# Kernel optimization log

Hardware: AMD Instinct MI355X
Metric: run time of the kernel (lower is better)

Reference implementation:

```python
import jax, jax.numpy as jnp
import numpy as np

B = 8       # number of point clouds
N = 4096    # points per cloud (start_point)
M = 1024    # sampled points per cloud (sampled_point_ammount), ratio 0.25
D = 64      # feature dim


def setup_inputs() -> dict:
    key = jax.random.key(0)
    k1, k2 = jax.random.split(key)
    x = jax.random.normal(k1, (B * N, D), dtype=jnp.float32)
    pos = jax.random.uniform(k2, (B * N, 3), dtype=jnp.float32)
    batch = jnp.repeat(jnp.arange(B, dtype=jnp.int32), N)  # sorted batch ids
    return {"x": x, "pos": pos, "batch": batch}


def _fps_single(pos_b, m):
    # Farthest point sampling on one cloud [N,3]; deterministic start at index 0.
    n = pos_b.shape[0]
    big = jnp.asarray(jnp.finfo(pos_b.dtype).max, pos_b.dtype)

    def step(carry, _):
        mind, last = carry
        d = jnp.sum((pos_b - pos_b[last]) ** 2, axis=-1)  # [N]
        mind = jnp.minimum(mind, d)
        nxt = jnp.argmax(mind).astype(jnp.int32)
        return (mind, nxt), nxt

    init = (jnp.full((n,), big, pos_b.dtype), jnp.int32(0))
    _, rest = jax.lax.scan(step, init, None, length=m - 1)
    return jnp.concatenate([jnp.zeros((1,), jnp.int32), rest])  # [M]


def reference(x, pos, batch):
    pos_b = pos.reshape(B, N, 3)
    # --- DownsampleMRG: FPS gather (scale_factor = M/N) ---
    idx = jax.vmap(lambda p: _fps_single(p, M))(pos_b)              # [B, M] local idx
    gidx = (idx + jnp.arange(B, dtype=jnp.int32)[:, None] * N).reshape(-1)
    x_lr = x[gidx]                                                  # [B*M, D]
    pos_lr = pos[gidx]                                              # [B*M, 3]
    # --- UpsampleMRG: lr_x = cat([x_lr, pos_lr]); knn_interpolate k=1 ---
    lr_feat = jnp.concatenate([x_lr, pos_lr], axis=1).reshape(B, M, D + 3)
    pos_lr_b = pos_lr.reshape(B, M, 3)
    # pairwise squared distances hr->lr within each cloud: [B, N, M]
    d2 = jnp.sum((pos_b[:, :, None, :] - pos_lr_b[:, None, :, :]) ** 2, axis=-1)
    nn = jnp.argmin(d2, axis=-1)                                    # [B, N]
    # k=1 interpolation: weights normalize to 1 -> pure nearest-neighbor gather
    interp = jnp.take_along_axis(lr_feat, nn[:, :, None], axis=1).reshape(B * N, D + 3)
    # out_x = cat([x_hr, pos_hr, interpolated lr features])
    out_x = jnp.concatenate([x, pos, interp], axis=1)               # [B*N, D+3+D+3]
    return out_x, jnp.zeros((out_x.shape[0], 3), pos.dtype), batch
```

## Files before the change

### kernel.cpp

```cpp
#include <hip/hip_runtime.h>
#include <cstdint>

#define BATCH 8
#define NPTS  4096
#define MPTS  1024
#define DIM   64

typedef float v2f __attribute__((ext_vector_type(2)));
typedef unsigned long long u64;
typedef unsigned int u32;

__device__ __forceinline__ double mk_key(float m, u32 aux) {
  const u64 k = ((u64)__float_as_uint(m) << 32) | (u64)aux;
  return __longlong_as_double((long long)k);
}
__device__ __forceinline__ u32 key_lo(double d) {
  return (u32)(u64)__double_as_longlong(d);
}

#define WAVE_MAX_F64_STEP(x, ctrl)                                                    \
  {                                                                                   \
    const u64 xu_ = (u64)__double_as_longlong(x);                                     \
    const int lo_ = __builtin_amdgcn_update_dpp(0, (int)(u32)xu_, (ctrl), 0xf, 0xf, true);  \
    const int hi_ = __builtin_amdgcn_update_dpp(0, (int)(u32)(xu_ >> 32), (ctrl), 0xf, 0xf, true); \
    const double y_ = __longlong_as_double((long long)(((u64)(u32)hi_ << 32) | (u64)(u32)lo_)); \
    (x) = fmax((x), y_);                                                              \
  }

__global__ __launch_bounds__(256) void fps_kernel(const float* __restrict__ pos,
                                                  int* __restrict__ gidx) {
#pragma clang fp contract(off)
  const int b = blockIdx.x;
  const int t = threadIdx.x;
  const float* p = pos + (size_t)b * NPTS * 3;

  __shared__ float4 sp[NPTS];
  __shared__ double red[2][4];

  v2f px[8], py[8], pz[8], mind[8];
#pragma unroll
  for (int k = 0; k < 16; ++k) {
    const int i = t + k * 256;
    const float a = p[3 * i + 0];
    const float c = p[3 * i + 1];
    const float d = p[3 * i + 2];
    sp[i] = make_float4(a, c, d, 0.0f);
    px[k >> 1][k & 1] = a;
    py[k >> 1][k & 1] = c;
    pz[k >> 1][k & 1] = d;
    mind[k >> 1][k & 1] = 3.402823466e+38f;
  }
  __syncthreads();

  float4 w = sp[0];
  float lx = w.x, ly = w.y, lz = w.z;

  int h0 = 0, h1 = 0, h2 = 0, h3 = 0;
  const int it1 = t + 256, it2 = t + 512, it3 = t + 768;

  for (int it = 1; it < MPTS; ++it) {
    const v2f vlx = {lx, lx}, vly = {ly, ly}, vlz = {lz, lz};
    double pg[8];
#pragma unroll
    for (int g = 0; g < 8; ++g) {
      const v2f dx = px[g] - vlx;
      const v2f dy = py[g] - vly;
      const v2f dz = pz[g] - vlz;
      const v2f d = (dx * dx + dy * dy) + dz * dz;
      const v2f m = __builtin_elementwise_min(mind[g], d);
      mind[g] = m;
      const double p0 = mk_key(m[0], ~(u32)(t + (2 * g) * 256));
      const double p1 = mk_key(m[1], ~(u32)(t + (2 * g + 1) * 256));
      pg[g] = fmax(p0, p1);
    }
    const double b0 = fmax(pg[0], pg[1]);
    const double b1 = fmax(pg[2], pg[3]);
    const double b2 = fmax(pg[4], pg[5]);
    const double b3 = fmax(pg[6], pg[7]);
    double best = fmax(fmax(b0, b1), fmax(b2, b3));

    WAVE_MAX_F64_STEP(best, 0x111);
    WAVE_MAX_F64_STEP(best, 0x112);
    WAVE_MAX_F64_STEP(best, 0x114);
    WAVE_MAX_F64_STEP(best, 0x118);
    WAVE_MAX_F64_STEP(best, 0x142);
    WAVE_MAX_F64_STEP(best, 0x143);

    const int buf = it & 1;
    if ((t & 63) == 63) red[buf][t >> 6] = best;
    __syncthreads();

    const double c = fmax(fmax(red[buf][0], red[buf][1]),
                          fmax(red[buf][2], red[buf][3]));
    const u32 widx = ~key_lo(c);

    w = sp[widx];
    lx = w.x; ly = w.y; lz = w.z;

    h0 = (it == t)   ? (int)widx : h0;
    h1 = (it == it1) ? (int)widx : h1;
    h2 = (it == it2) ? (int)widx : h2;
    h3 = (it == it3) ? (int)widx : h3;
  }

  const int base = b * MPTS;
  const int goff = b * NPTS;
  gidx[base + t]       = goff + h0;
  gidx[base + 256 + t] = goff + h1;
  gidx[base + 512 + t] = goff + h2;
  gidx[base + 768 + t] = goff + h3;
}

__global__ __launch_bounds__(256) void nn_kernel(const float* __restrict__ pos,
                                                 const int* __restrict__ gidx,
                                                 int* __restrict__ nng) {
#pragma clang fp contract(off)
  const int b = blockIdx.x >> 5;
  const int chunk = blockIdx.x & 31;
  const int t = threadIdx.x;

  __shared__ float lrx[MPTS], lry[MPTS], lrz[MPTS];
  for (int j = t; j < MPTS; j += 256) {
    const int g = gidx[b * MPTS + j];
    lrx[j] = pos[3 * g + 0];
    lry[j] = pos[3 * g + 1];
    lrz[j] = pos[3 * g + 2];
  }
  __syncthreads();

  const int pt = chunk * 128 + (t >> 1);
  const int half = t & 1;
  const int i = b * NPTS + pt;
  const float x = pos[3 * i + 0];
  const float y = pos[3 * i + 1];
  const float z = pos[3 * i + 2];
  const v2f vx = {x, x}, vy = {y, y}, vz = {z, z};

  double best = __longlong_as_double(0x7FEFFFFFFFFFFFFFll);
  const int j0 = half * 512;
#pragma unroll 4
  for (int s = 0; s < 256; ++s) {
    const int j = j0 + 2 * s;
    const v2f qx = *(const v2f*)&lrx[j];
    const v2f qy = *(const v2f*)&lry[j];
    const v2f qz = *(const v2f*)&lrz[j];
    const v2f dx = vx - qx;
    const v2f dy = vy - qy;
    const v2f dz = vz - qz;
    const v2f d = (dx * dx + dy * dy) + dz * dz;
    const double p0 = mk_key(d[0], (u32)j);
    const double p1 = mk_key(d[1], (u32)(j + 1));
    best = fmin(best, fmin(p0, p1));
  }
  const u64 bu = (u64)__double_as_longlong(best);
  const u64 ou = ((u64)(u32)__shfl_xor((int)(bu >> 32), 1, 64) << 32) |
                 (u64)(u32)__shfl_xor((int)(u32)bu, 1, 64);
  best = fmin(best, __longlong_as_double((long long)ou));
  if (half == 0) nng[i] = gidx[b * MPTS + (int)key_lo(best)];
}

__global__ __launch_bounds__(256) void assemble_kernel(const float* __restrict__ x,
                                                       const float* __restrict__ pos,
                                                       const int* __restrict__ batch,
                                                       const int* __restrict__ nng,
                                                       float* __restrict__ out) {
  const int w = (int)((blockIdx.x * 256 + threadIdx.x) >> 6);
  const int lane = threadIdx.x & 63;
  if (w >= BATCH * NPTS) return;
  const int g = nng[w];

  float* o = out + (size_t)w * 134;
  o[lane] = x[(size_t)w * DIM + lane];
  o[67 + lane] = x[(size_t)g * DIM + lane];
  if (lane < 3) {
    o[64 + lane] = pos[3 * w + lane];
    o[131 + lane] = pos[3 * g + lane];
  }

  float* o2 = out + (size_t)BATCH * NPTS * 134;
  if (lane < 3) o2[3 * w + lane] = 0.0f;
  float* o3 = o2 + (size_t)BATCH * NPTS * 3;
  if (lane == 0) o3[w] = (float)batch[w];
}

extern "C" void kernel_launch(void* const* d_in, const int* in_sizes, int n_in,
                              void* d_out, int out_size, void* d_ws, size_t ws_size,
                              hipStream_t stream) {
  const float* x = (const float*)d_in[0];
  const float* pos = (const float*)d_in[1];
  const int* batch = (const int*)d_in[2];

  int* gidx = (int*)d_ws;
  int* nng = gidx + BATCH * MPTS;

  float* out = (float*)d_out;

  fps_kernel<<<BATCH, 256, 0, stream>>>(pos, gidx);
  nn_kernel<<<BATCH * 32, 256, 0, stream>>>(pos, gidx, nng);
  assemble_kernel<<<(BATCH * NPTS * 64) / 256, 256, 0, stream>>>(x, pos, batch, nng, out);
}
```

Before: 561.4 us.

## Split FPS argmax into f32 value reduction then u32 index reduction

Replaces the per-element 64-bit packed (distance,index) fmax keys in the FPS loop with a 32-bit float max tree plus a branch-free selection of the winning slot index, followed by a float DPP wave max using readlanes, then a separate u32 DPP max over candidate indices. This avoids the 64-bit packing and double-precision max ops and halves the DPP traffic for the value reduction. In exchange it adds a second wave reduction pass and selection logic, and tie-breaking must still match the lowest index.

```diff
diff --git a/kernel.cpp b/kernel.cpp
--- a/kernel.cpp
+++ b/kernel.cpp
@@ -17,14 +17,18 @@
 __device__ __forceinline__ u32 key_lo(double d) {
   return (u32)(u64)__double_as_longlong(d);
 }
-
-#define WAVE_MAX_F64_STEP(x, ctrl)                                                    \
+__device__ __forceinline__ u32 umax_(u32 a, u32 b) { return a > b ? a : b; }
+
+#define WAVE_MAX_F32_STEP(x, ctrl)                                                    \
   {                                                                                   \
-    const u64 xu_ = (u64)__double_as_longlong(x);                                     \
-    const int lo_ = __builtin_amdgcn_update_dpp(0, (int)(u32)xu_, (ctrl), 0xf, 0xf, true);  \
-    const int hi_ = __builtin_amdgcn_update_dpp(0, (int)(u32)(xu_ >> 32), (ctrl), 0xf, 0xf, true); \
-    const double y_ = __longlong_as_double((long long)(((u64)(u32)hi_ << 32) | (u64)(u32)lo_)); \
-    (x) = fmax((x), y_);                                                              \
+    const int y_ = __builtin_amdgcn_update_dpp(0, __float_as_int(x), (ctrl), 0xf, 0xf, true); \
+    (x) = fmaxf((x), __int_as_float(y_));                                             \
+  }
+
+#define WAVE_MAX_U32_STEP(x, ctrl)                                                    \
+  {                                                                                   \
+    const int y_ = __builtin_amdgcn_update_dpp(0, (int)(x), (ctrl), 0xf, 0xf, true);  \
+    (x) = umax_((x), (u32)y_);                                                        \
   }
 
 __global__ __launch_bounds__(256) void fps_kernel(const float* __restrict__ pos,
@@ -60,34 +64,67 @@
 
   for (int it = 1; it < MPTS; ++it) {
     const v2f vlx = {lx, lx}, vly = {ly, ly}, vlz = {lz, lz};
-    double pg[8];
 #pragma unroll
     for (int g = 0; g < 8; ++g) {
       const v2f dx = px[g] - vlx;
       const v2f dy = py[g] - vly;
       const v2f dz = pz[g] - vlz;
       const v2f d = (dx * dx + dy * dy) + dz * dz;
-      const v2f m = __builtin_elementwise_min(mind[g], d);
-      mind[g] = m;
-      const double p0 = mk_key(m[0], ~(u32)(t + (2 * g) * 256));
-      const double p1 = mk_key(m[1], ~(u32)(t + (2 * g + 1) * 256));
-      pg[g] = fmax(p0, p1);
+      mind[g] = __builtin_elementwise_min(mind[g], d);
     }
-    const double b0 = fmax(pg[0], pg[1]);
-    const double b1 = fmax(pg[2], pg[3]);
-    const double b2 = fmax(pg[4], pg[5]);
-    const double b3 = fmax(pg[6], pg[7]);
-    double best = fmax(fmax(b0, b1), fmax(b2, b3));
-
-    WAVE_MAX_F64_STEP(best, 0x111);
-    WAVE_MAX_F64_STEP(best, 0x112);
-    WAVE_MAX_F64_STEP(best, 0x114);
-    WAVE_MAX_F64_STEP(best, 0x118);
-    WAVE_MAX_F64_STEP(best, 0x142);
-    WAVE_MAX_F64_STEP(best, 0x143);
+
+    const float v0 = mind[0][0], v1 = mind[0][1], v2 = mind[1][0], v3 = mind[1][1];
+    const float v4 = mind[2][0], v5 = mind[2][1], v6 = mind[3][0], v7 = mind[3][1];
+    const float v8 = mind[4][0], v9 = mind[4][1], v10 = mind[5][0], v11 = mind[5][1];
+    const float v12 = mind[6][0], v13 = mind[6][1], v14 = mind[7][0], v15 = mind[7][1];
+    const float a0 = fmaxf(v0, v1),  a1 = fmaxf(v2, v3);
+    const float a2 = fmaxf(v4, v5),  a3 = fmaxf(v6, v7);
+    const float a4 = fmaxf(v8, v9),  a5 = fmaxf(v10, v11);
+    const float a6 = fmaxf(v12, v13), a7 = fmaxf(v14, v15);
+    const float b0 = fmaxf(a0, a1), b1 = fmaxf(a2, a3);
+    const float b2 = fmaxf(a4, a5), b3 = fmaxf(a6, a7);
+    const float c0 = fmaxf(b0, b1), c1 = fmaxf(b2, b3);
+    const float m16 = fmaxf(c0, c1);
+
+    const bool e3 = (c0 == m16);
+    const float bL = e3 ? b0 : b2;
+    const bool e2 = (bL == m16);
+    const float aLt = e3 ? a0 : a4;
+    const float aLf = e3 ? a2 : a6;
+    const float aL = e2 ? aLt : aLf;
+    const bool e1 = (aL == m16);
+    const float q0 = e1 ? v0 : v2,  q1 = e1 ? v4 : v6;
+    const float q2 = e1 ? v8 : v10, q3 = e1 ? v12 : v14;
+    const float q4 = e2 ? q0 : q1,  q5 = e2 ? q2 : q3;
+    const float vL = e3 ? q4 : q5;
+    const bool e0 = (vL == m16);
+    const int kk = (e3 ? 0 : 8) | (e2 ? 0 : 4) | (e1 ? 0 : 2) | (e0 ? 0 : 1);
+    const u32 myc = ~((u32)t + ((u32)kk << 8));
+
+    float pm = m16;
+    WAVE_MAX_F32_STEP(pm, 0x111);
+    WAVE_MAX_F32_STEP(pm, 0x112);
+    WAVE_MAX_F32_STEP(pm, 0x114);
+    WAVE_MAX_F32_STEP(pm, 0x118);
+    const int pmb = __float_as_int(pm);
+    const u32 r0 = (u32)__builtin_amdgcn_readlane(pmb, 15);
+    const u32 r1 = (u32)__builtin_amdgcn_readlane(pmb, 31);
+    const u32 r2 = (u32)__builtin_amdgcn_readlane(pmb, 47);
+    const u32 r3 = (u32)__builtin_amdgcn_readlane(pmb, 63);
+    const u32 wv = umax_(umax_(r0, r1), umax_(r2, r3));
+
+    u32 cand = (__float_as_uint(m16) == wv) ? myc : 0u;
+    WAVE_MAX_U32_STEP(cand, 0x111);
+    WAVE_MAX_U32_STEP(cand, 0x112);
+    WAVE_MAX_U32_STEP(cand, 0x114);
+    WAVE_MAX_U32_STEP(cand, 0x118);
+    WAVE_MAX_U32_STEP(cand, 0x142);
+    WAVE_MAX_U32_STEP(cand, 0x143);
 
     const int buf = it & 1;
-    if ((t & 63) == 63) red[buf][t >> 6] = best;
+    if ((t & 63) == 63)
+      red[buf][t >> 6] =
+          __longlong_as_double((long long)(((u64)wv << 32) | (u64)cand));
     __syncthreads();
 
     const double c = fmax(fmax(red[buf][0], red[buf][1]),
```

Measured after the change: 604.2 us. 1.08x slower.

## Carry winner coordinates through FPS reduction and fuse NN search with output assembly

Applied to the files above, without the earlier changes.

In the FPS loop, each lane prefetches its candidate point's coordinates from shared memory before the wave reduction. The lane holding the wave maximum publishes both key and coordinates, so the block-level selection no longer needs a dependent shared-memory load on the critical serial path. Separately, the nearest-neighbour kernel and the assemble kernel are merged, so each point's output row is written right after its neighbour is found, removing a launch and the nng round trip. The fused assembly uses per-thread row copies with strided, less coalesced stores, which may cost bandwidth compared with the previous one-wave-per-row layout.

```diff
diff --git a/kernel.cpp b/kernel.cpp
--- a/kernel.cpp
+++ b/kernel.cpp
@@ -35,7 +35,8 @@
   const float* p = pos + (size_t)b * NPTS * 3;
 
   __shared__ float4 sp[NPTS];
-  __shared__ double red[2][4];
+  __shared__ double sK[2][4];
+  __shared__ float4 sA[2][4];
 
   v2f px[8], py[8], pz[8], mind[8];
 #pragma unroll
@@ -54,6 +55,7 @@
 
   float4 w = sp[0];
   float lx = w.x, ly = w.y, lz = w.z;
+  const int wid = t >> 6;
 
   int h0 = 0, h1 = 0, h2 = 0, h3 = 0;
   const int it1 = t + 256, it2 = t + 512, it3 = t + 768;
@@ -77,25 +79,42 @@
     const double b1 = fmax(pg[2], pg[3]);
     const double b2 = fmax(pg[4], pg[5]);
     const double b3 = fmax(pg[6], pg[7]);
-    double best = fmax(fmax(b0, b1), fmax(b2, b3));
-
-    WAVE_MAX_F64_STEP(best, 0x111);
-    WAVE_MAX_F64_STEP(best, 0x112);
-    WAVE_MAX_F64_STEP(best, 0x114);
-    WAVE_MAX_F64_STEP(best, 0x118);
-    WAVE_MAX_F64_STEP(best, 0x142);
-    WAVE_MAX_F64_STEP(best, 0x143);
+    const double best = fmax(fmax(b0, b1), fmax(b2, b3));
+
+    const u32 ow = ~key_lo(best);
+    const float4 wc = sp[ow];
+
+    double wm = best;
+    WAVE_MAX_F64_STEP(wm, 0x111);
+    WAVE_MAX_F64_STEP(wm, 0x112);
+    WAVE_MAX_F64_STEP(wm, 0x114);
+    WAVE_MAX_F64_STEP(wm, 0x118);
+    WAVE_MAX_F64_STEP(wm, 0x142);
+    WAVE_MAX_F64_STEP(wm, 0x143);
+
+    const u64 wmb = (u64)__double_as_longlong(wm);
+    const u32 mhi = (u32)__builtin_amdgcn_readlane((int)(u32)(wmb >> 32), 63);
+    const u32 mlo = (u32)__builtin_amdgcn_readlane((int)(u32)wmb, 63);
+    const u64 wmax = ((u64)mhi << 32) | (u64)mlo;
 
     const int buf = it & 1;
-    if ((t & 63) == 63) red[buf][t >> 6] = best;
+    if ((u64)__double_as_longlong(best) == wmax) {
+      sK[buf][wid] = best;
+      sA[buf][wid] = wc;
+    }
     __syncthreads();
 
-    const double c = fmax(fmax(red[buf][0], red[buf][1]),
-                          fmax(red[buf][2], red[buf][3]));
+    const double k0 = sK[buf][0], k1 = sK[buf][1], k2 = sK[buf][2], k3 = sK[buf][3];
+    const float4 a0 = sA[buf][0], a1 = sA[buf][1], a2 = sA[buf][2], a3 = sA[buf][3];
+    const double c01 = fmax(k0, k1), c23 = fmax(k2, k3);
+    const double c = fmax(c01, c23);
+    const bool s1 = (c01 == k1);
+    const bool s3 = (c23 == k3);
+    const bool sh = (c == c23);
+    const float ux = s1 ? a1.x : a0.x, uy = s1 ? a1.y : a0.y, uz = s1 ? a1.z : a0.z;
+    const float vx2 = s3 ? a3.x : a2.x, vy2 = s3 ? a3.y : a2.y, vz2 = s3 ? a3.z : a2.z;
+    lx = sh ? vx2 : ux; ly = sh ? vy2 : uy; lz = sh ? vz2 : uz;
     const u32 widx = ~key_lo(c);
-
-    w = sp[widx];
-    lx = w.x; ly = w.y; lz = w.z;
 
     h0 = (it == t)   ? (int)widx : h0;
     h1 = (it == it1) ? (int)widx : h1;
@@ -111,15 +130,18 @@
   gidx[base + 768 + t] = goff + h3;
 }
 
-__global__ __launch_bounds__(256) void nn_kernel(const float* __restrict__ pos,
-                                                 const int* __restrict__ gidx,
-                                                 int* __restrict__ nng) {
+__global__ __launch_bounds__(256) void nn_assemble_kernel(
+    const float* __restrict__ x, const float* __restrict__ pos,
+    const int* __restrict__ batch, const int* __restrict__ gidx,
+    float* __restrict__ out) {
 #pragma clang fp contract(off)
   const int b = blockIdx.x >> 5;
   const int chunk = blockIdx.x & 31;
   const int t = threadIdx.x;
 
   __shared__ float lrx[MPTS], lry[MPTS], lrz[MPTS];
+  __shared__ int snn[128];
+
   for (int j = t; j < MPTS; j += 256) {
     const int g = gidx[b * MPTS + j];
     lrx[j] = pos[3 * g + 0];
@@ -128,13 +150,13 @@
   }
   __syncthreads();
 
-  const int pt = chunk * 128 + (t >> 1);
+  const int r = t >> 1;
   const int half = t & 1;
-  const int i = b * NPTS + pt;
-  const float x = pos[3 * i + 0];
-  const float y = pos[3 * i + 1];
-  const float z = pos[3 * i + 2];
-  const v2f vx = {x, x}, vy = {y, y}, vz = {z, z};
+  const int i = b * NPTS + chunk * 128 + r;
+  const float X = pos[3 * i + 0];
+  const float Y = pos[3 * i + 1];
+  const float Z = pos[3 * i + 2];
+  const v2f vX = {X, X}, vY = {Y, Y}, vZ = {Z, Z};
 
   double best = __longlong_as_double(0x7FEFFFFFFFFFFFFFll);
   const int j0 = half * 512;
@@ -144,9 +166,9 @@
     const v2f qx = *(const v2f*)&lrx[j];
     const v2f qy = *(const v2f*)&lry[j];
     const v2f qz = *(const v2f*)&lrz[j];
-    const v2f dx = vx - qx;
-    const v2f dy = vy - qy;
-    const v2f dz = vz - qz;
+    const v2f dx = vX - qx;
+    const v2f dy = vY - qy;
+    const v2f dz = vZ - qz;
     const v2f d = (dx * dx + dy * dy) + dz * dz;
     const double p0 = mk_key(d[0], (u32)j);
     const double p1 = mk_key(d[1], (u32)(j + 1));
@@ -156,31 +178,42 @@
   const u64 ou = ((u64)(u32)__shfl_xor((int)(bu >> 32), 1, 64) << 32) |
                  (u64)(u32)__shfl_xor((int)(u32)bu, 1, 64);
   best = fmin(best, __longlong_as_double((long long)ou));
-  if (half == 0) nng[i] = gidx[b * MPTS + (int)key_lo(best)];
-}
-
-__global__ __launch_bounds__(256) void assemble_kernel(const float* __restrict__ x,
-                                                       const float* __restrict__ pos,
-                                                       const int* __restrict__ batch,
-                                                       const int* __restrict__ nng,
-                                                       float* __restrict__ out) {
-  const int w = (int)((blockIdx.x * 256 + threadIdx.x) >> 6);
-  const int lane = threadIdx.x & 63;
-  if (w >= BATCH * NPTS) return;
-  const int g = nng[w];
-
-  float* o = out + (size_t)w * 134;
-  o[lane] = x[(size_t)w * DIM + lane];
-  o[67 + lane] = x[(size_t)g * DIM + lane];
-  if (lane < 3) {
-    o[64 + lane] = pos[3 * w + lane];
-    o[131 + lane] = pos[3 * g + lane];
-  }
-
-  float* o2 = out + (size_t)BATCH * NPTS * 134;
-  if (lane < 3) o2[3 * w + lane] = 0.0f;
-  float* o3 = o2 + (size_t)BATCH * NPTS * 3;
-  if (lane == 0) o3[w] = (float)batch[w];
+  if (half == 0) snn[r] = gidx[b * MPTS + (int)key_lo(best)];
+  __syncthreads();
+
+  const int g = snn[r];
+  float* o = out + (size_t)i * 134;
+  if (half == 0) {
+    const float4* xr = (const float4*)(x + (size_t)i * DIM);
+#pragma unroll
+    for (int q = 0; q < 16; ++q) {
+      const float4 v = xr[q];
+      *(v2f*)(o + 4 * q)     = v2f{v.x, v.y};
+      *(v2f*)(o + 4 * q + 2) = v2f{v.z, v.w};
+    }
+    o[64] = X; o[65] = Y; o[66] = Z;
+    float* o2 = out + (size_t)BATCH * NPTS * 134 + (size_t)i * 3;
+    o2[0] = 0.0f; o2[1] = 0.0f; o2[2] = 0.0f;
+  } else {
+    const float4* xg = (const float4*)(x + (size_t)g * DIM);
+    float e[64];
+#pragma unroll
+    for (int q = 0; q < 16; ++q) {
+      const float4 v = xg[q];
+      e[4 * q + 0] = v.x; e[4 * q + 1] = v.y;
+      e[4 * q + 2] = v.z; e[4 * q + 3] = v.w;
+    }
+    o[67] = e[0];
+#pragma unroll
+    for (int m = 0; m < 31; ++m)
+      *(v2f*)(o + 68 + 2 * m) = v2f{e[2 * m + 1], e[2 * m + 2]};
+    o[130] = e[63];
+    o[131] = pos[3 * g + 0];
+    o[132] = pos[3 * g + 1];
+    o[133] = pos[3 * g + 2];
+    float* o3 = out + (size_t)BATCH * NPTS * 134 + (size_t)BATCH * NPTS * 3;
+    o3[i] = (float)batch[i];
+  }
 }
 
 extern "C" void kernel_launch(void* const* d_in, const int* in_sizes, int n_in,
@@ -191,11 +224,9 @@
   const int* batch = (const int*)d_in[2];
 
   int* gidx = (int*)d_ws;
-  int* nng = gidx + BATCH * MPTS;
 
   float* out = (float*)d_out;
 
   fps_kernel<<<BATCH, 256, 0, stream>>>(pos, gidx);
-  nn_kernel<<<BATCH * 32, 256, 0, stream>>>(pos, gidx, nng);
-  assemble_kernel<<<(BATCH * NPTS * 64) / 256, 256, 0, stream>>>(x, pos, batch, nng, out);
-}
+  nn_assemble_kernel<<<BATCH * 32, 256, 0, stream>>>(x, pos, batch, gidx, out);
+}
```

Measured after the change: 677.0 us. 20.6% more time.
